# Optimization experiments

Measured on AMD Instinct MI355X. Metric: run time of the kernel, lower is better.

The kernel has to match this reference:

```python
import jax, jax.numpy as jnp
import numpy as np

LN_EPS = 1e-5  # torch.nn.LayerNorm default


def setup_inputs() -> dict:
    key = jax.random.key(0)
    k1, k2, k3 = jax.random.split(key, 3)
    B, N, F, D = 8, 2048, 128, 128
    A_hat = jax.random.uniform(k1, (B, N, N), dtype=jnp.float32)
    X = jax.random.normal(k2, (B, N, F), dtype=jnp.float32)
    W = jax.random.normal(k3, (D, F), dtype=jnp.float32) * (1.0 / np.sqrt(F))
    b = jnp.zeros((D,), dtype=jnp.float32)
    gamma = jnp.ones((D,), dtype=jnp.float32)
    beta = jnp.zeros((D,), dtype=jnp.float32)
    return {"A_hat": A_hat, "X": X, "W": W, "b": b, "gamma": gamma, "beta": beta}


def reference(A_hat, X, W, b, gamma, beta):
    # batched aggregation: H[b] = A_hat[b] @ X[b]   (torch loop over batch, vectorized here)
    H = jnp.einsum('bnm,bmf->bnf', A_hat, X)
    # linear: torch nn.Linear stores W as [out, in]
    H = jnp.einsum('bnf,df->bnd', H, W) + b
    # LayerNorm over last dim, then ReLU (dropout p=0 -> identity)
    mu = jnp.mean(H, axis=-1, keepdims=True)
    var = jnp.mean((H - mu) ** 2, axis=-1, keepdims=True)
    Hn = (H - mu) * jax.lax.rsqrt(var + LN_EPS) * gamma + beta
    return jax.nn.relu(Hn)
```

## Files before the change

kernel.cpp:

```cpp
#include <hip/hip_runtime.h>
#include <stdint.h>

#define B_DIM 8
#define N_DIM 2048
#define F_DIM 128
#define LN_EPS 1e-5f

typedef __attribute__((ext_vector_type(8))) short short8;
typedef __attribute__((ext_vector_type(4))) float floatx4;

__device__ __forceinline__ ushort f2bf(float f) {
    union { float f; uint32_t u; } c;
    c.f = f;
    uint32_t u = c.u;
    return (ushort)((u + 0x7FFFu + ((u >> 16) & 1u)) >> 16);
}

__device__ __forceinline__ uint32_t pk2bf(float a, float b) {
    union { float f; uint32_t u; } x, y;
    x.f = a; y.f = b;
    return ((x.u + 0x8000u) >> 16) | ((y.u + 0x8000u) & 0xFFFF0000u);
}

__device__ __forceinline__ short8 pack8(float4 lo, float4 hi) {
    union { uint32_t u[4]; short8 s; } r;
    r.u[0] = pk2bf(lo.x, lo.y);
    r.u[1] = pk2bf(lo.z, lo.w);
    r.u[2] = pk2bf(hi.x, hi.y);
    r.u[3] = pk2bf(hi.z, hi.w);
    return r.s;
}

__device__ __forceinline__ void load_lds16(const ushort* g, ushort* l) {
    __builtin_amdgcn_global_load_lds(
        (const __attribute__((address_space(1))) void*)g,
        (__attribute__((address_space(3))) void*)l,
        16, 0, 0);
}

__global__ __launch_bounds__(256) void k_transpose(const float* __restrict__ X,
                                                   ushort* __restrict__ Xt) {
    __shared__ ushort tile[64 * 65];
    const int t = threadIdx.x;
    const int b = blockIdx.z;
    const int k0 = blockIdx.x * 64;
    const int f0 = blockIdx.y * 64;

#pragma unroll
    for (int p = 0; p < 2; ++p) {
        int idx = p * 256 + t;
        int kk = idx >> 3;
        int ff = (idx & 7) * 8;
        const float* src = X + (((size_t)b * N_DIM) + k0 + kk) * F_DIM + f0 + ff;
        float4 v0 = *(const float4*)(src);
        float4 v1 = *(const float4*)(src + 4);
        ushort* d = tile + kk * 65 + ff;
        d[0] = f2bf(v0.x); d[1] = f2bf(v0.y); d[2] = f2bf(v0.z); d[3] = f2bf(v0.w);
        d[4] = f2bf(v1.x); d[5] = f2bf(v1.y); d[6] = f2bf(v1.z); d[7] = f2bf(v1.w);
    }
    __syncthreads();

    union U { uint4 v; ushort s[8]; };
#pragma unroll
    for (int p = 0; p < 2; ++p) {
        int idx = p * 256 + t;
        int f2 = idx >> 3;
        int kk2 = (idx & 7) * 8;
        U u;
#pragma unroll
        for (int j = 0; j < 8; ++j) u.s[j] = tile[(kk2 + j) * 65 + f2];
        *(uint4*)(Xt + (((size_t)b * F_DIM) + f0 + f2) * N_DIM + k0 + kk2) = u.v;
    }
}

__global__ __launch_bounds__(256) void k_fused(const float* __restrict__ A,
                                               const ushort* __restrict__ Xt,
                                               const float* __restrict__ W,
                                               const float* __restrict__ bias,
                                               const float* __restrict__ gamma,
                                               const float* __restrict__ beta,
                                               float* __restrict__ out) {
    __shared__ __align__(16) char smem[81920];
    ushort* const As0 = (ushort*)smem;
    ushort* const As1 = (ushort*)(smem + 8192);
    ushort* const Bs0 = (ushort*)(smem + 16384);
    ushort* const Bs1 = (ushort*)(smem + 16384 + 32768);
    ushort* const Ht = (ushort*)smem;
    float (*const Pt)[132] = (float(*)[132])(smem + 16384);

    const int t = threadIdx.x;
    const int lane = t & 63;
    const int w = t >> 6;
    const int q = lane >> 4;
    const int mr = lane & 15;

    const int bid = blockIdx.x;
    const int bb = bid & 7;
    const int m0 = (bid >> 3) * 32;

    const float* Ab = A + ((size_t)bb * N_DIM + m0) * N_DIM;
    const ushort* Xb = Xt + (size_t)bb * F_DIM * N_DIM;

    const int arow = t >> 3;
    const int asw_ = arow & 7;
    const float* a_src = Ab + (size_t)arow * N_DIM + (t & 7) * 16;
    const int a_off0 = arow * 128 + ((((t & 7) * 2) ^ asw_) * 8);
    const int a_off1 = arow * 128 + ((((t & 7) * 2 + 1) ^ asw_) * 8);

    const ushort* b_src[8];
    int b_off[8];
#pragma unroll
    for (int p = 0; p < 8; ++p) {
        int c = p * 256 + t;
        int n = c >> 4;
        int kc = (c & 15) ^ (n & 7);
        b_src[p] = Xb + (size_t)n * N_DIM + kc * 8;
        b_off[p] = c * 8;
    }

    floatx4 acc[2][2];
#pragma unroll
    for (int i = 0; i < 2; ++i)
#pragma unroll
        for (int j = 0; j < 2; ++j) acc[i][j] = (floatx4){0.f, 0.f, 0.f, 0.f};

    auto stageB = [&](int k0, ushort* Bn) {
#pragma unroll
        for (int p = 0; p < 8; ++p) load_lds16(b_src[p] + k0, Bn + b_off[p]);
    };
    auto packA = [&](float4 v0, float4 v1, float4 v2, float4 v3, ushort* An) {
        *(short8*)(An + a_off0) = pack8(v0, v1);
        *(short8*)(An + a_off1) = pack8(v2, v3);
    };
    auto compute = [&](const ushort* Ac, const ushort* Bc) {
#pragma unroll
        for (int ks = 0; ks < 4; ++ks) {
            short8 af[2], bfr[2];
#pragma unroll
            for (int i = 0; i < 2; ++i) {
                int m = mr + i * 16;
                af[i] = *(const short8*)(Ac + m * 128 + (((ks * 4 + q) ^ (m & 7)) * 8));
            }
#pragma unroll
            for (int j = 0; j < 2; ++j) {
                int n = w * 32 + j * 16 + mr;
                bfr[j] = *(const short8*)(Bc + n * 128 + (((ks * 4 + q) ^ (n & 7)) * 8));
            }
#pragma unroll
            for (int i = 0; i < 2; ++i)
#pragma unroll
                for (int j = 0; j < 2; ++j)
                    acc[i][j] = __builtin_amdgcn_mfma_f32_16x16x32_bf16(
                        af[i], bfr[j], acc[i][j], 0, 0, 0);
        }
    };

    float4 r0a, r0b, r0c, r0d, r1a, r1b, r1c, r1d;

    {
        const float4* ap = (const float4*)(a_src);
        r0a = ap[0]; r0b = ap[1]; r0c = ap[2]; r0d = ap[3];
        stageB(0, Bs0);
        packA(r0a, r0b, r0c, r0d, As0);
        __builtin_amdgcn_sched_barrier(0);
        const float4* ap1 = (const float4*)(a_src + 128);
        r1a = ap1[0]; r1b = ap1[1]; r1c = ap1[2]; r1d = ap1[3];
    }
    asm volatile("s_waitcnt vmcnt(4) lgkmcnt(0)" ::: "memory");
    __builtin_amdgcn_s_barrier();

#pragma unroll 1
    for (int tt = 0; tt < 14; tt += 2) {
        const int k0 = tt * 128;
        stageB(k0 + 128, Bs1);
        __builtin_amdgcn_sched_barrier(0);
        {
            const float4* ap = (const float4*)(a_src + k0 + 256);
            r0a = ap[0]; r0b = ap[1]; r0c = ap[2]; r0d = ap[3];
        }
        compute(As0, Bs0);
        packA(r1a, r1b, r1c, r1d, As1);
        asm volatile("s_waitcnt vmcnt(4) lgkmcnt(0)" ::: "memory");
        __builtin_amdgcn_s_barrier();

        stageB(k0 + 256, Bs0);
        __builtin_amdgcn_sched_barrier(0);
        {
            const float4* ap = (const float4*)(a_src + k0 + 384);
            r1a = ap[0]; r1b = ap[1]; r1c = ap[2]; r1d = ap[3];
        }
        compute(As1, Bs1);
        packA(r0a, r0b, r0c, r0d, As0);
        asm volatile("s_waitcnt vmcnt(4) lgkmcnt(0)" ::: "memory");
        __builtin_amdgcn_s_barrier();
    }

    stageB(15 * 128, Bs1);
    compute(As0, Bs0);
    packA(r1a, r1b, r1c, r1d, As1);
    asm volatile("s_waitcnt vmcnt(0) lgkmcnt(0)" ::: "memory");
    __builtin_amdgcn_s_barrier();

    compute(As1, Bs1);
    __syncthreads();

#pragma unroll
    for (int j = 0; j < 2; ++j) {
        int col = w * 32 + j * 16 + mr;
#pragma unroll
        for (int r = 0; r < 4; ++r) {
            Ht[(q * 4 + r) * 136 + col] = f2bf(acc[0][j][r]);
            Ht[(16 + q * 4 + r) * 136 + col] = f2bf(acc[1][j][r]);
        }
    }
    __syncthreads();

    floatx4 p[2][2];
#pragma unroll
    for (int i = 0; i < 2; ++i)
#pragma unroll
        for (int j = 0; j < 2; ++j) p[i][j] = (floatx4){0.f, 0.f, 0.f, 0.f};

#pragma unroll
    for (int ks = 0; ks < 4; ++ks) {
        short8 ha0 = *(const short8*)(Ht + mr * 136 + ks * 32 + q * 8);
        short8 ha1 = *(const short8*)(Ht + (mr + 16) * 136 + ks * 32 + q * 8);
#pragma unroll
        for (int j = 0; j < 2; ++j) {
            const float* wp = W + (w * 32 + j * 16 + mr) * F_DIM + ks * 32 + q * 8;
            short8 wb = pack8(((const float4*)wp)[0], ((const float4*)wp)[1]);
            p[0][j] = __builtin_amdgcn_mfma_f32_16x16x32_bf16(ha0, wb, p[0][j], 0, 0, 0);
            p[1][j] = __builtin_amdgcn_mfma_f32_16x16x32_bf16(ha1, wb, p[1][j], 0, 0, 0);
        }
    }

#pragma unroll
    for (int j = 0; j < 2; ++j) {
        int col = w * 32 + j * 16 + mr;
        float bcol = bias[col];
#pragma unroll
        for (int r = 0; r < 4; ++r) {
            Pt[q * 4 + r][col] = p[0][j][r] + bcol;
            Pt[16 + q * 4 + r][col] = p[1][j][r] + bcol;
        }
    }
    __syncthreads();

    const int row = t >> 3;
    const int seg = t & 7;
    float v[16];
    float s = 0.f, s2 = 0.f;
#pragma unroll
    for (int u = 0; u < 16; ++u) {
        v[u] = Pt[row][seg * 16 + u];
        s += v[u];
        s2 += v[u] * v[u];
    }
    s += __shfl_xor(s, 1);  s2 += __shfl_xor(s2, 1);
    s += __shfl_xor(s, 2);  s2 += __shfl_xor(s2, 2);
    s += __shfl_xor(s, 4);  s2 += __shfl_xor(s2, 4);
    float mu = s * (1.0f / 128.0f);
    float var = s2 * (1.0f / 128.0f) - mu * mu;
    float rs = rsqrtf(var + LN_EPS);

    float4 o[4];
    float* of = (float*)o;
#pragma unroll
    for (int u = 0; u < 16; ++u) {
        int d = seg * 16 + u;
        float y = (v[u] - mu) * rs * gamma[d] + beta[d];
        of[u] = fmaxf(y, 0.0f);
    }
    float4* dst = (float4*)(out + ((size_t)bb * N_DIM + m0 + row) * F_DIM + seg * 16);
    dst[0] = o[0]; dst[1] = o[1]; dst[2] = o[2]; dst[3] = o[3];
}

extern "C" void kernel_launch(void* const* d_in, const int* in_sizes, int n_in,
                              void* d_out, int out_size, void* d_ws, size_t ws_size,
                              hipStream_t stream) {
    const float* A     = (const float*)d_in[0];
    const float* X     = (const float*)d_in[1];
    const float* W     = (const float*)d_in[2];
    const float* bias  = (const float*)d_in[3];
    const float* gamma = (const float*)d_in[4];
    const float* beta  = (const float*)d_in[5];
    float* out = (float*)d_out;

    ushort* Xt = (ushort*)d_ws;

    k_transpose<<<dim3(32, 2, 8), 256, 0, stream>>>(X, Xt);
    k_fused<<<dim3(512), 256, 0, stream>>>(A, Xt, W, bias, gamma, beta, out);
}
```

Before: 210.9 us.

## Halve row tile and K-step to shrink LDS and double grid occupancy

Rows per block drop from 32 to 16 and the K step from 128 to 64, which cuts LDS use from 80KB to 36KB and doubles the grid to 1024 blocks. Launch bounds now request 4 blocks per CU. On 256 CUs the old 512-block grid left some CUs with a single block, and this change aims to raise occupancy and latency hiding for the A stream. In exchange, the X tiles are reloaded twice as often per output row, which doubles total B traffic from L2. There are also twice as many barriers per unit of work, and fewer MFMAs run per LDS read.

```diff
diff --git a/kernel.cpp b/kernel.cpp
--- a/kernel.cpp
+++ b/kernel.cpp
@@ -73,20 +73,20 @@
     }
 }
 
-__global__ __launch_bounds__(256) void k_fused(const float* __restrict__ A,
-                                               const ushort* __restrict__ Xt,
-                                               const float* __restrict__ W,
-                                               const float* __restrict__ bias,
-                                               const float* __restrict__ gamma,
-                                               const float* __restrict__ beta,
-                                               float* __restrict__ out) {
-    __shared__ __align__(16) char smem[81920];
+__global__ __launch_bounds__(256, 4) void k_fused(const float* __restrict__ A,
+                                                  const ushort* __restrict__ Xt,
+                                                  const float* __restrict__ W,
+                                                  const float* __restrict__ bias,
+                                                  const float* __restrict__ gamma,
+                                                  const float* __restrict__ beta,
+                                                  float* __restrict__ out) {
+    __shared__ __align__(16) char smem[36864];
     ushort* const As0 = (ushort*)smem;
-    ushort* const As1 = (ushort*)(smem + 8192);
-    ushort* const Bs0 = (ushort*)(smem + 16384);
-    ushort* const Bs1 = (ushort*)(smem + 16384 + 32768);
+    ushort* const As1 = (ushort*)(smem + 2048);
+    ushort* const Bs0 = (ushort*)(smem + 4096);
+    ushort* const Bs1 = (ushort*)(smem + 4096 + 16384);
     ushort* const Ht = (ushort*)smem;
-    float (*const Pt)[132] = (float(*)[132])(smem + 16384);
+    float (*const Pt)[132] = (float(*)[132])(smem + 9216);
 
     const int t = threadIdx.x;
     const int lane = t & 63;
@@ -96,108 +96,89 @@
 
     const int bid = blockIdx.x;
     const int bb = bid & 7;
-    const int m0 = (bid >> 3) * 32;
+    const int m0 = (bid >> 3) * 16;
 
     const float* Ab = A + ((size_t)bb * N_DIM + m0) * N_DIM;
     const ushort* Xb = Xt + (size_t)bb * F_DIM * N_DIM;
 
-    const int arow = t >> 3;
-    const int asw_ = arow & 7;
-    const float* a_src = Ab + (size_t)arow * N_DIM + (t & 7) * 16;
-    const int a_off0 = arow * 128 + ((((t & 7) * 2) ^ asw_) * 8);
-    const int a_off1 = arow * 128 + ((((t & 7) * 2 + 1) ^ asw_) * 8);
-
-    const ushort* b_src[8];
-    int b_off[8];
-#pragma unroll
-    for (int p = 0; p < 8; ++p) {
+    const int arow = t >> 4;
+    const float* a_src = Ab + (size_t)arow * N_DIM + (t & 15) * 4;
+    const int a_off = arow * 64 + (((t & 15) >> 1) ^ (arow & 7)) * 8 + (t & 1) * 4;
+
+    const ushort* b_src[4];
+    int b_off[4];
+#pragma unroll
+    for (int p = 0; p < 4; ++p) {
         int c = p * 256 + t;
-        int n = c >> 4;
-        int kc = (c & 15) ^ (n & 7);
+        int n = c >> 3;
+        int kc = (c & 7) ^ (n & 7);
         b_src[p] = Xb + (size_t)n * N_DIM + kc * 8;
         b_off[p] = c * 8;
     }
 
-    floatx4 acc[2][2];
-#pragma unroll
-    for (int i = 0; i < 2; ++i)
-#pragma unroll
-        for (int j = 0; j < 2; ++j) acc[i][j] = (floatx4){0.f, 0.f, 0.f, 0.f};
+    floatx4 acc[2];
+    acc[0] = (floatx4){0.f, 0.f, 0.f, 0.f};
+    acc[1] = (floatx4){0.f, 0.f, 0.f, 0.f};
 
     auto stageB = [&](int k0, ushort* Bn) {
 #pragma unroll
-        for (int p = 0; p < 8; ++p) load_lds16(b_src[p] + k0, Bn + b_off[p]);
+        for (int p = 0; p < 4; ++p) load_lds16(b_src[p] + k0, Bn + b_off[p]);
     };
-    auto packA = [&](float4 v0, float4 v1, float4 v2, float4 v3, ushort* An) {
-        *(short8*)(An + a_off0) = pack8(v0, v1);
-        *(short8*)(An + a_off1) = pack8(v2, v3);
+    auto packA = [&](float4 v, ushort* An) {
+        union { uint32_t u[2]; } r;
+        r.u[0] = pk2bf(v.x, v.y);
+        r.u[1] = pk2bf(v.z, v.w);
+        *(uint2*)(An + a_off) = *(const uint2*)r.u;
     };
     auto compute = [&](const ushort* Ac, const ushort* Bc) {
 #pragma unroll
-        for (int ks = 0; ks < 4; ++ks) {
-            short8 af[2], bfr[2];
-#pragma unroll
-            for (int i = 0; i < 2; ++i) {
-                int m = mr + i * 16;
-                af[i] = *(const short8*)(Ac + m * 128 + (((ks * 4 + q) ^ (m & 7)) * 8));
-            }
+        for (int ks = 0; ks < 2; ++ks) {
+            short8 af = *(const short8*)(Ac + mr * 64 +
+                                         (((ks * 4 + q) ^ (mr & 7)) * 8));
 #pragma unroll
             for (int j = 0; j < 2; ++j) {
                 int n = w * 32 + j * 16 + mr;
-                bfr[j] = *(const short8*)(Bc + n * 128 + (((ks * 4 + q) ^ (n & 7)) * 8));
+                short8 bfr = *(const short8*)(Bc + n * 64 +
+                                              (((ks * 4 + q) ^ (n & 7)) * 8));
+                acc[j] = __builtin_amdgcn_mfma_f32_16x16x32_bf16(af, bfr, acc[j],
+                                                                 0, 0, 0);
             }
-#pragma unroll
-            for (int i = 0; i < 2; ++i)
-#pragma unroll
-                for (int j = 0; j < 2; ++j)
-                    acc[i][j] = __builtin_amdgcn_mfma_f32_16x16x32_bf16(
-                        af[i], bfr[j], acc[i][j], 0, 0, 0);
         }
     };
 
-    float4 r0a, r0b, r0c, r0d, r1a, r1b, r1c, r1d;
-
-    {
-        const float4* ap = (const float4*)(a_src);
-        r0a = ap[0]; r0b = ap[1]; r0c = ap[2]; r0d = ap[3];
-        stageB(0, Bs0);
-        packA(r0a, r0b, r0c, r0d, As0);
+    float4 r0, r1;
+
+    r0 = *(const float4*)(a_src);
+    stageB(0, Bs0);
+    packA(r0, As0);
+    __builtin_amdgcn_sched_barrier(0);
+    r1 = *(const float4*)(a_src + 64);
+    asm volatile("s_waitcnt vmcnt(1) lgkmcnt(0)" ::: "memory");
+    __builtin_amdgcn_s_barrier();
+
+#pragma unroll 1
+    for (int tt = 0; tt < 30; tt += 2) {
+        const int k0 = tt * 64;
+        stageB(k0 + 64, Bs1);
         __builtin_amdgcn_sched_barrier(0);
-        const float4* ap1 = (const float4*)(a_src + 128);
-        r1a = ap1[0]; r1b = ap1[1]; r1c = ap1[2]; r1d = ap1[3];
-    }
-    asm volatile("s_waitcnt vmcnt(4) lgkmcnt(0)" ::: "memory");
-    __builtin_amdgcn_s_barrier();
-
-#pragma unroll 1
-    for (int tt = 0; tt < 14; tt += 2) {
-        const int k0 = tt * 128;
-        stageB(k0 + 128, Bs1);
+        r0 = *(const float4*)(a_src + k0 + 128);
+        compute(As0, Bs0);
+        packA(r1, As1);
+        asm volatile("s_waitcnt vmcnt(1) lgkmcnt(0)" ::: "memory");
+        __builtin_amdgcn_s_barrier();
+
+        stageB(k0 + 128, Bs0);
         __builtin_amdgcn_sched_barrier(0);
-        {
-            const float4* ap = (const float4*)(a_src + k0 + 256);
-            r0a = ap[0]; r0b = ap[1]; r0c = ap[2]; r0d = ap[3];
-        }
-        compute(As0, Bs0);
-        packA(r1a, r1b, r1c, r1d, As1);
-        asm volatile("s_waitcnt vmcnt(4) lgkmcnt(0)" ::: "memory");
+        r1 = *(const float4*)(a_src + k0 + 192);
+        compute(As1, Bs1);
+        packA(r0, As0);
+        asm volatile("s_waitcnt vmcnt(1) lgkmcnt(0)" ::: "memory");
         __builtin_amdgcn_s_barrier();
-
-        stageB(k0 + 256, Bs0);
-        __builtin_amdgcn_sched_barrier(0);
-        {
-            const float4* ap = (const float4*)(a_src + k0 + 384);
-            r1a = ap[0]; r1b = ap[1]; r1c = ap[2]; r1d = ap[3];
-        }
-        compute(As1, Bs1);
-        packA(r0a, r0b, r0c, r0d, As0);
-        asm volatile("s_waitcnt vmcnt(4) lgkmcnt(0)" ::: "memory");
-        __builtin_amdgcn_s_barrier();
-    }
-
-    stageB(15 * 128, Bs1);
+    }
+
+    stageB(31 * 64, Bs1);
     compute(As0, Bs0);
-    packA(r1a, r1b, r1c, r1d, As1);
+    packA(r1, As1);
     asm volatile("s_waitcnt vmcnt(0) lgkmcnt(0)" ::: "memory");
     __builtin_amdgcn_s_barrier();
 
@@ -208,29 +189,23 @@
     for (int j = 0; j < 2; ++j) {
         int col = w * 32 + j * 16 + mr;
 #pragma unroll
-        for (int r = 0; r < 4; ++r) {
-            Ht[(q * 4 + r) * 136 + col] = f2bf(acc[0][j][r]);
-            Ht[(16 + q * 4 + r) * 136 + col] = f2bf(acc[1][j][r]);
-        }
-    }
-    __syncthreads();
-
-    floatx4 p[2][2];
-#pragma unroll
-    for (int i = 0; i < 2; ++i)
-#pragma unroll
-        for (int j = 0; j < 2; ++j) p[i][j] = (floatx4){0.f, 0.f, 0.f, 0.f};
+        for (int r = 0; r < 4; ++r)
+            Ht[(q * 4 + r) * 136 + col] = f2bf(acc[j][r]);
+    }
+    __syncthreads();
+
+    floatx4 p[2];
+    p[0] = (floatx4){0.f, 0.f, 0.f, 0.f};
+    p[1] = (floatx4){0.f, 0.f, 0.f, 0.f};
 
 #pragma unroll
     for (int ks = 0; ks < 4; ++ks) {
-        short8 ha0 = *(const short8*)(Ht + mr * 136 + ks * 32 + q * 8);
-        short8 ha1 = *(const short8*)(Ht + (mr + 16) * 136 + ks * 32 + q * 8);
+        short8 ha = *(const short8*)(Ht + mr * 136 + ks * 32 + q * 8);
 #pragma unroll
         for (int j = 0; j < 2; ++j) {
             const float* wp = W + (w * 32 + j * 16 + mr) * F_DIM + ks * 32 + q * 8;
             short8 wb = pack8(((const float4*)wp)[0], ((const float4*)wp)[1]);
-            p[0][j] = __builtin_amdgcn_mfma_f32_16x16x32_bf16(ha0, wb, p[0][j], 0, 0, 0);
-            p[1][j] = __builtin_amdgcn_mfma_f32_16x16x32_bf16(ha1, wb, p[1][j], 0, 0, 0);
+            p[j] = __builtin_amdgcn_mfma_f32_16x16x32_bf16(ha, wb, p[j], 0, 0, 0);
         }
     }
 
@@ -239,40 +214,39 @@
         int col = w * 32 + j * 16 + mr;
         float bcol = bias[col];
 #pragma unroll
-        for (int r = 0; r < 4; ++r) {
-            Pt[q * 4 + r][col] = p[0][j][r] + bcol;
-            Pt[16 + q * 4 + r][col] = p[1][j][r] + bcol;
-        }
-    }
-    __syncthreads();
-
-    const int row = t >> 3;
-    const int seg = t & 7;
-    float v[16];
+        for (int r = 0; r < 4; ++r)
+            Pt[q * 4 + r][col] = p[j][r] + bcol;
+    }
+    __syncthreads();
+
+    const int row = t >> 4;
+    const int seg = t & 15;
+    float v[8];
     float s = 0.f, s2 = 0.f;
 #pragma unroll
-    for (int u = 0; u < 16; ++u) {
-        v[u] = Pt[row][seg * 16 + u];
+    for (int u = 0; u < 8; ++u) {
+        v[u] = Pt[row][seg * 8 + u];
         s += v[u];
         s2 += v[u] * v[u];
     }
     s += __shfl_xor(s, 1);  s2 += __shfl_xor(s2, 1);
     s += __shfl_xor(s, 2);  s2 += __shfl_xor(s2, 2);
     s += __shfl_xor(s, 4);  s2 += __shfl_xor(s2, 4);
+    s += __shfl_xor(s, 8);  s2 += __shfl_xor(s2, 8);
     float mu = s * (1.0f / 128.0f);
     float var = s2 * (1.0f / 128.0f) - mu * mu;
     float rs = rsqrtf(var + LN_EPS);
 
-    float4 o[4];
+    float4 o[2];
     float* of = (float*)o;
 #pragma unroll
-    for (int u = 0; u < 16; ++u) {
-        int d = seg * 16 + u;
+    for (int u = 0; u < 8; ++u) {
+        int d = seg * 8 + u;
         float y = (v[u] - mu) * rs * gamma[d] + beta[d];
         of[u] = fmaxf(y, 0.0f);
     }
-    float4* dst = (float4*)(out + ((size_t)bb * N_DIM + m0 + row) * F_DIM + seg * 16);
-    dst[0] = o[0]; dst[1] = o[1]; dst[2] = o[2]; dst[3] = o[3];
+    float4* dst = (float4*)(out + ((size_t)bb * N_DIM + m0 + row) * F_DIM + seg * 8);
+    dst[0] = o[0]; dst[1] = o[1];
 }
 
 extern "C" void kernel_launch(void* const* d_in, const int* in_sizes, int n_in,
@@ -289,5 +263,5 @@
     ushort* Xt = (ushort*)d_ws;
 
     k_transpose<<<dim3(32, 2, 8), 256, 0, stream>>>(X, Xt);
-    k_fused<<<dim3(512), 256, 0, stream>>>(A, Xt, W, bias, gamma, beta, out);
-}
+    k_fused<<<dim3(1024), 256, 0, stream>>>(A, Xt, W, bias, gamma, beta, out);
+}
```

Result: slower. 226.4 us (+7.3%).

## Reassociate to A@(X·Wᵀ) and precompute transposed XWᵀ in prep kernel

Applied to the files above, without the earlier changes.

Uses associativity to compute Y = X·Wᵀ once per batch in a prep kernel, which also writes the transposed bf16 layout, so the main kernel does A@Y directly. This removes the per-tile second GEMM, its LDS round trip through Ht and a barrier from the fused kernel. It also adds launch_bounds(256,2) as an occupancy hint. The cost is an extra bf16 rounding of Y before aggregation, which slightly changes numerics, and prep now does a small GEMM instead of a pure transpose.

```diff
diff --git a/kernel.cpp b/kernel.cpp
--- a/kernel.cpp
+++ b/kernel.cpp
@@ -38,55 +38,83 @@
         16, 0, 0);
 }
 
-__global__ __launch_bounds__(256) void k_transpose(const float* __restrict__ X,
-                                                   ushort* __restrict__ Xt) {
-    __shared__ ushort tile[64 * 65];
+__global__ __launch_bounds__(256) void k_prep(const float* __restrict__ X,
+                                              const float* __restrict__ W,
+                                              ushort* __restrict__ Yt) {
+    __shared__ __align__(16) ushort Xs[64 * 128];
     const int t = threadIdx.x;
-    const int b = blockIdx.z;
-    const int k0 = blockIdx.x * 64;
-    const int f0 = blockIdx.y * 64;
-
-#pragma unroll
-    for (int p = 0; p < 2; ++p) {
-        int idx = p * 256 + t;
-        int kk = idx >> 3;
-        int ff = (idx & 7) * 8;
-        const float* src = X + (((size_t)b * N_DIM) + k0 + kk) * F_DIM + f0 + ff;
-        float4 v0 = *(const float4*)(src);
-        float4 v1 = *(const float4*)(src + 4);
-        ushort* d = tile + kk * 65 + ff;
-        d[0] = f2bf(v0.x); d[1] = f2bf(v0.y); d[2] = f2bf(v0.z); d[3] = f2bf(v0.w);
-        d[4] = f2bf(v1.x); d[5] = f2bf(v1.y); d[6] = f2bf(v1.z); d[7] = f2bf(v1.w);
+    const int lane = t & 63;
+    const int w = t >> 6;
+    const int q = lane >> 4;
+    const int mr = lane & 15;
+
+    const int b = blockIdx.x >> 5;
+    const int k0 = (blockIdx.x & 31) * 64;
+
+    const int r = t >> 2;
+    const int f0 = (t & 3) * 32;
+    const float* src = X + (((size_t)b * N_DIM) + k0 + r) * F_DIM + f0;
+    float4 v[8];
+#pragma unroll
+    for (int p = 0; p < 8; ++p) v[p] = ((const float4*)src)[p];
+#pragma unroll
+    for (int c2 = 0; c2 < 4; ++c2) {
+        int chunk = (f0 >> 3) + c2;
+        *(short8*)(Xs + r * 128 + ((chunk ^ (r & 7)) * 8)) =
+            pack8(v[2 * c2], v[2 * c2 + 1]);
     }
     __syncthreads();
 
-    union U { uint4 v; ushort s[8]; };
-#pragma unroll
-    for (int p = 0; p < 2; ++p) {
-        int idx = p * 256 + t;
-        int f2 = idx >> 3;
-        int kk2 = (idx & 7) * 8;
-        U u;
-#pragma unroll
-        for (int j = 0; j < 8; ++j) u.s[j] = tile[(kk2 + j) * 65 + f2];
-        *(uint4*)(Xt + (((size_t)b * F_DIM) + f0 + f2) * N_DIM + k0 + kk2) = u.v;
-    }
-}
-
-__global__ __launch_bounds__(256) void k_fused(const float* __restrict__ A,
-                                               const ushort* __restrict__ Xt,
-                                               const float* __restrict__ W,
-                                               const float* __restrict__ bias,
-                                               const float* __restrict__ gamma,
-                                               const float* __restrict__ beta,
-                                               float* __restrict__ out) {
+    floatx4 acc[4][2];
+#pragma unroll
+    for (int i = 0; i < 4; ++i)
+#pragma unroll
+        for (int j = 0; j < 2; ++j) acc[i][j] = (floatx4){0.f, 0.f, 0.f, 0.f};
+
+#pragma unroll
+    for (int ks = 0; ks < 4; ++ks) {
+        short8 af[4];
+#pragma unroll
+        for (int i = 0; i < 4; ++i) {
+            int m = i * 16 + mr;
+            af[i] = *(const short8*)(Xs + m * 128 + (((ks * 4 + q) ^ (m & 7)) * 8));
+        }
+#pragma unroll
+        for (int j = 0; j < 2; ++j) {
+            const float* wp = W + (w * 32 + j * 16 + mr) * F_DIM + ks * 32 + q * 8;
+            short8 wb = pack8(((const float4*)wp)[0], ((const float4*)wp)[1]);
+#pragma unroll
+            for (int i = 0; i < 4; ++i)
+                acc[i][j] = __builtin_amdgcn_mfma_f32_16x16x32_bf16(af[i], wb,
+                                                                    acc[i][j], 0, 0, 0);
+        }
+    }
+
+#pragma unroll
+    for (int i = 0; i < 4; ++i)
+#pragma unroll
+        for (int j = 0; j < 2; ++j) {
+            int d = w * 32 + j * 16 + mr;
+            union { ushort s[4]; uint2 u; } o;
+#pragma unroll
+            for (int r2 = 0; r2 < 4; ++r2) o.s[r2] = f2bf(acc[i][j][r2]);
+            *(uint2*)(Yt + (((size_t)b * F_DIM) + d) * N_DIM + k0 + i * 16 + q * 4) =
+                o.u;
+        }
+}
+
+__global__ __launch_bounds__(256, 2) void k_fused(const float* __restrict__ A,
+                                                  const ushort* __restrict__ Yt,
+                                                  const float* __restrict__ bias,
+                                                  const float* __restrict__ gamma,
+                                                  const float* __restrict__ beta,
+                                                  float* __restrict__ out) {
     __shared__ __align__(16) char smem[81920];
     ushort* const As0 = (ushort*)smem;
     ushort* const As1 = (ushort*)(smem + 8192);
     ushort* const Bs0 = (ushort*)(smem + 16384);
     ushort* const Bs1 = (ushort*)(smem + 16384 + 32768);
-    ushort* const Ht = (ushort*)smem;
-    float (*const Pt)[132] = (float(*)[132])(smem + 16384);
+    float (*const Pt)[132] = (float(*)[132])smem;
 
     const int t = threadIdx.x;
     const int lane = t & 63;
@@ -99,7 +127,7 @@
     const int m0 = (bid >> 3) * 32;
 
     const float* Ab = A + ((size_t)bb * N_DIM + m0) * N_DIM;
-    const ushort* Xb = Xt + (size_t)bb * F_DIM * N_DIM;
+    const ushort* Yb = Yt + (size_t)bb * F_DIM * N_DIM;
 
     const int arow = t >> 3;
     const int asw_ = arow & 7;
@@ -114,7 +142,7 @@
         int c = p * 256 + t;
         int n = c >> 4;
         int kc = (c & 15) ^ (n & 7);
-        b_src[p] = Xb + (size_t)n * N_DIM + kc * 8;
+        b_src[p] = Yb + (size_t)n * N_DIM + kc * 8;
         b_off[p] = c * 8;
     }
 
@@ -207,41 +235,11 @@
 #pragma unroll
     for (int j = 0; j < 2; ++j) {
         int col = w * 32 + j * 16 + mr;
+        float bcol = bias[col];
 #pragma unroll
         for (int r = 0; r < 4; ++r) {
-            Ht[(q * 4 + r) * 136 + col] = f2bf(acc[0][j][r]);
-            Ht[(16 + q * 4 + r) * 136 + col] = f2bf(acc[1][j][r]);
-        }
-    }
-    __syncthreads();
-
-    floatx4 p[2][2];
-#pragma unroll
-    for (int i = 0; i < 2; ++i)
-#pragma unroll
-        for (int j = 0; j < 2; ++j) p[i][j] = (floatx4){0.f, 0.f, 0.f, 0.f};
-
-#pragma unroll
-    for (int ks = 0; ks < 4; ++ks) {
-        short8 ha0 = *(const short8*)(Ht + mr * 136 + ks * 32 + q * 8);
-        short8 ha1 = *(const short8*)(Ht + (mr + 16) * 136 + ks * 32 + q * 8);
-#pragma unroll
-        for (int j = 0; j < 2; ++j) {
-            const float* wp = W + (w * 32 + j * 16 + mr) * F_DIM + ks * 32 + q * 8;
-            short8 wb = pack8(((const float4*)wp)[0], ((const float4*)wp)[1]);
-            p[0][j] = __builtin_amdgcn_mfma_f32_16x16x32_bf16(ha0, wb, p[0][j], 0, 0, 0);
-            p[1][j] = __builtin_amdgcn_mfma_f32_16x16x32_bf16(ha1, wb, p[1][j], 0, 0, 0);
-        }
-    }
-
-#pragma unroll
-    for (int j = 0; j < 2; ++j) {
-        int col = w * 32 + j * 16 + mr;
-        float bcol = bias[col];
-#pragma unroll
-        for (int r = 0; r < 4; ++r) {
-            Pt[q * 4 + r][col] = p[0][j][r] + bcol;
-            Pt[16 + q * 4 + r][col] = p[1][j][r] + bcol;
+            Pt[q * 4 + r][col] = acc[0][j][r] + bcol;
+            Pt[16 + q * 4 + r][col] = acc[1][j][r] + bcol;
         }
     }
     __syncthreads();
@@ -286,8 +284,8 @@
     const float* beta  = (const float*)d_in[5];
     float* out = (float*)d_out;
 
-    ushort* Xt = (ushort*)d_ws;
-
-    k_transpose<<<dim3(32, 2, 8), 256, 0, stream>>>(X, Xt);
-    k_fused<<<dim3(512), 256, 0, stream>>>(A, Xt, W, bias, gamma, beta, out);
-}
+    ushort* Yt = (ushort*)d_ws;
+
+    k_prep<<<dim3(256), 256, 0, stream>>>(X, W, Yt);
+    k_fused<<<dim3(512), 256, 0, stream>>>(A, Yt, bias, gamma, beta, out);
+}
```

Result: no change. 214.4 us (+1.6%).
